# Optimization experiments

Measured on AMD Instinct MI355X. Metric: run time of the kernel, lower is better.

The kernel has to match this reference:

```python
import jax, jax.numpy as jnp
import numpy as np

B, T, C, H = 2, 2048, 1024, 16
HD = C // H  # head_dim = 64


def _apply_rope(x, cos, sin):
    # x: [B, T, H, HD]; cos/sin: [T, HD//2]
    xp = x.reshape(x.shape[:-1] + (HD // 2, 2))  # [B,T,H,HD//2,2]
    x0, x1 = xp[..., 0], xp[..., 1]
    c = cos[None, :, None, :]
    s = sin[None, :, None, :]
    rot = jnp.stack([x0 * c - x1 * s, x0 * s + x1 * c], axis=-1)
    return rot.reshape(x.shape)


def setup_inputs() -> dict:
    key0 = jax.random.key(0)
    ks = jax.random.split(key0, 8)
    query = jax.random.normal(ks[0], (B, T, C), dtype=jnp.float32)
    key_ = jax.random.normal(ks[1], (B, T, C), dtype=jnp.float32)
    value = jax.random.normal(ks[2], (B, T, C), dtype=jnp.float32)
    # standard RoPE angle table: pos * inv_freq, shape [T, HD//2]
    pos = jnp.arange(T, dtype=jnp.float32)
    inv_freq = 1.0 / (10000.0 ** (jnp.arange(0, HD, 2, dtype=jnp.float32) / HD))
    freqs = pos[:, None] * inv_freq[None, :]
    scale = 0.02
    Wq = jax.random.normal(ks[3], (C, C), dtype=jnp.float32) * scale
    Wk = jax.random.normal(ks[4], (C, C), dtype=jnp.float32) * scale
    Wv = jax.random.normal(ks[5], (C, C), dtype=jnp.float32) * scale
    Wo = jax.random.normal(ks[6], (C, C), dtype=jnp.float32) * scale
    return {"query": query, "key": key_, "value": value, "freqs": freqs,
            "Wq": Wq, "Wk": Wk, "Wv": Wv, "Wo": Wo}


def reference(query, key, value, freqs, Wq, Wk, Wv, Wo):
    # torch nn.Linear: y = x @ W.T (no bias)
    Q = query @ Wq.T
    K = key @ Wk.T
    V = value @ Wv.T
    cos = jnp.cos(freqs)
    sin = jnp.sin(freqs)
    Q = _apply_rope(Q.reshape(B, T, H, HD), cos, sin)
    K = _apply_rope(K.reshape(B, T, H, HD), cos, sin)
    V = V.reshape(B, T, H, HD)
    # non-causal SDPA, scale = 1/sqrt(head_dim)
    scores = jnp.einsum('bthd,bshd->bhts', Q, K) / jnp.sqrt(jnp.float32(HD))
    probs = jax.nn.softmax(scores, axis=-1)
    y = jnp.einsum('bhts,bshd->bthd', probs, V).reshape(B, T, C)
    return y @ Wo.T
```

## Files before the change

### kernel.cpp

```cpp
#include <hip/hip_runtime.h>
#include <stdint.h>

#define Bd 2
#define Td 2048
#define Cd 1024
#define Hd 16
#define HDd 64
#define BT 4096

typedef _Float16 f16;
typedef __attribute__((ext_vector_type(8))) _Float16 f16x8;
typedef __attribute__((ext_vector_type(4))) _Float16 f16x4;
typedef __attribute__((ext_vector_type(2))) _Float16 f16x2;
typedef __attribute__((ext_vector_type(4))) float f32x4;
typedef __attribute__((ext_vector_type(16))) float f32x16;
typedef __attribute__((ext_vector_type(2))) unsigned uint2v;

#define GLD_LDS16(gptr, lptr)                                                        \
    __builtin_amdgcn_global_load_lds((const __attribute__((address_space(1))) void*)(gptr), \
                                     (__attribute__((address_space(3))) void*)(lptr), 16, 0, 0)

#define MAX3(a, b, c) fmaxf(fmaxf(a, b), c)
#define EXP2(x) __builtin_amdgcn_exp2f(x)

__device__ __forceinline__ float2 xhalf_pair(float v) {
    uint2v r = __builtin_amdgcn_permlane32_swap(__float_as_uint(v), __float_as_uint(v), false, false);
    unsigned lo = r[0], hi = r[1];
    float2 out;
    out.x = __uint_as_float(lo);
    out.y = __uint_as_float(hi);
    return out;
}

__global__ void k_cvt(const float* __restrict__ q, const float* __restrict__ k,
                      const float* __restrict__ v, const float* __restrict__ wq,
                      const float* __restrict__ wk, const float* __restrict__ wv,
                      const float* __restrict__ wo, f16* __restrict__ qh, f16* __restrict__ kh,
                      f16* __restrict__ vh, f16* __restrict__ wqh, f16* __restrict__ wkh,
                      f16* __restrict__ wvh, f16* __restrict__ woh,
                      const float* __restrict__ freqs, float2* __restrict__ csT) {
    int g = blockIdx.x * 256 + threadIdx.x;
    if (g >= 4194304) {
        int i = g - 4194304;
        float f = freqs[i];
        float2 cs;
        cs.x = cosf(f);
        cs.y = sinf(f);
        csT[i] = cs;
        return;
    }
    const float* src;
    f16* dst;
    int base;
    if (g < 1048576)      { src = q;  dst = qh;  base = 0; }
    else if (g < 2097152) { src = k;  dst = kh;  base = 1048576; }
    else if (g < 3145728) { src = v;  dst = vh;  base = 2097152; }
    else if (g < 3407872) { src = wq; dst = wqh; base = 3145728; }
    else if (g < 3670016) { src = wk; dst = wkh; base = 3407872; }
    else if (g < 3932160) { src = wv; dst = wvh; base = 3670016; }
    else                  { src = wo; dst = woh; base = 3932160; }
    int i = g - base;
    float4 val = reinterpret_cast<const float4*>(src)[i];
    f16x4 o;
    o[0] = (f16)val.x; o[1] = (f16)val.y; o[2] = (f16)val.z; o[3] = (f16)val.w;
    reinterpret_cast<f16x4*>(dst)[i] = o;
}

#define GEMM_MAINLOOP(A, W)                                                                  \
    const int tid = threadIdx.x;                                                             \
    const int lane = tid & 63, w = tid >> 6;                                                 \
    const int g = lane >> 4, r15 = lane & 15;                                                \
    const int m0 = blockIdx.x * 128, n0 = blockIdx.y * 128;                                  \
    const int wm = (w >> 1) * 64, wn = (w & 1) * 64;                                         \
    const f32x4 zero4 = {0.f, 0.f, 0.f, 0.f};                                                \
    f32x4 acc[4][4];                                                                         \
    _Pragma("unroll") for (int i = 0; i < 4; ++i) {                                          \
        _Pragma("unroll") for (int j = 0; j < 4; ++j) acc[i][j] = zero4;                     \
    }                                                                                        \
    const int srow0 = tid >> 3;                                                              \
    const int sj = tid & 7;                                                                  \
    for (int k0 = 0; k0 < Cd; k0 += 64) {                                                    \
        _Pragma("unroll") for (int c = 0; c < 4; ++c) {                                      \
            int row = c * 32 + srow0;                                                        \
            int ch = sj ^ (row & 7);                                                         \
            GLD_LDS16(A + (m0 + row) * Cd + k0 + ch * 8, Alds + (c * 256 + w * 64) * 8);     \
            GLD_LDS16(W + (n0 + row) * Cd + k0 + ch * 8, Blds + (c * 256 + w * 64) * 8);     \
        }                                                                                    \
        __syncthreads();                                                                     \
        _Pragma("unroll") for (int half = 0; half < 2; ++half) {                             \
            f16x8 af[4], bf[4];                                                              \
            _Pragma("unroll") for (int t = 0; t < 4; ++t) {                                  \
                int cidx = ((half << 2) | g) ^ (r15 & 7);                                    \
                af[t] = *(const f16x8*)&Alds[(wm + t * 16 + r15) * 64 + cidx * 8];           \
                bf[t] = *(const f16x8*)&Blds[(wn + t * 16 + r15) * 64 + cidx * 8];           \
            }                                                                                \
            _Pragma("unroll") for (int i = 0; i < 4; ++i) {                                  \
                _Pragma("unroll") for (int j = 0; j < 4; ++j) acc[i][j] =                    \
                    __builtin_amdgcn_mfma_f32_16x16x32_f16(af[i], bf[j], acc[i][j], 0, 0, 0); \
            }                                                                                \
        }                                                                                    \
        __syncthreads();                                                                     \
    }

__global__ __launch_bounds__(256, 3) void k_gemm_qkv(
    const f16* __restrict__ qh, const f16* __restrict__ kh, const f16* __restrict__ vh,
    const f16* __restrict__ wqh, const f16* __restrict__ wkh, const f16* __restrict__ wvh,
    f16* __restrict__ Qp, f16* __restrict__ Kp, f16* __restrict__ Vt,
    const float2* __restrict__ csT) {
    __shared__ __attribute__((aligned(16))) char smem[34816];
    f16* Alds = (f16*)smem;
    f16* Blds = (f16*)(smem + 16384);
    const int z = blockIdx.z;
    const f16* A = (z == 0) ? qh : (z == 1) ? kh : vh;
    const f16* W = (z == 0) ? wqh : (z == 1) ? wkh : wvh;
    GEMM_MAINLOOP(A, W)
    if (z < 2) {
        f16* outp = z ? Kp : Qp;
#pragma unroll
        for (int i = 0; i < 4; ++i) {
#pragma unroll
            for (int j = 0; j < 4; ++j) {
#pragma unroll
                for (int r = 0; r < 4; ++r) {
                    int row = m0 + wm + i * 16 + g * 4 + r;
                    int col = n0 + wn + j * 16 + r15;
                    float own = acc[i][j][r];
                    float par = __shfl_xor(own, 1, 64);
                    float2 cs = csT[(row & 2047) * 32 + ((j * 16 + r15) >> 1)];
                    float val = (r15 & 1) ? fmaf(par, cs.y, own * cs.x)
                                          : fmaf(own, cs.x, -par * cs.y);
                    outp[row * Cd + col] = (f16)val;
                }
            }
        }
    } else {
        f16* Clds = (f16*)smem;
#pragma unroll
        for (int i = 0; i < 4; ++i) {
#pragma unroll
            for (int j = 0; j < 4; ++j) {
                f16x4 pv;
#pragma unroll
                for (int r = 0; r < 4; ++r) pv[r] = (f16)acc[i][j][r];
                *(f16x4*)&Clds[(wn + j * 16 + r15) * 136 + wm + i * 16 + g * 4] = pv;
            }
        }
        __syncthreads();
        const int orow = tid >> 1;
        const int th = (tid & 1) * 64;
        const int gcol = n0 + orow;
        const int hh = gcol >> 6, dd = gcol & 63;
        const int bb = m0 >> 11;
        f16* dst = Vt + ((bb * 16 + hh) * 64 + dd) * 2048 + (m0 & 2047) + th;
#pragma unroll
        for (int c = 0; c < 8; ++c) {
            f16x8 vv = *(const f16x8*)&Clds[orow * 136 + th + c * 8];
            *(f16x8*)&dst[c * 8] = vv;
        }
    }
}

__global__ __launch_bounds__(256, 4) void k_gemm_out(const f16* __restrict__ yh,
                                                     const f16* __restrict__ woh,
                                                     float* __restrict__ out) {
    __shared__ __attribute__((aligned(16))) f16 Alds[128 * 64];
    __shared__ __attribute__((aligned(16))) f16 Blds[64 * 64];
    const int tid = threadIdx.x;
    const int lane = tid & 63, w = tid >> 6;
    const int g = lane >> 4, r15 = lane & 15;
    const int m0 = blockIdx.x * 128, n0 = blockIdx.y * 64;
    const int wm = (w >> 1) * 64, wn = (w & 1) * 32;
    const f32x4 zero4 = {0.f, 0.f, 0.f, 0.f};
    f32x4 acc[4][2];
#pragma unroll
    for (int i = 0; i < 4; ++i) {
#pragma unroll
        for (int j = 0; j < 2; ++j) acc[i][j] = zero4;
    }
    const int srow0 = tid >> 3;
    const int sj = tid & 7;
    for (int k0 = 0; k0 < Cd; k0 += 64) {
#pragma unroll
        for (int c = 0; c < 4; ++c) {
            int row = c * 32 + srow0;
            int ch = sj ^ (row & 7);
            GLD_LDS16(yh + (m0 + row) * Cd + k0 + ch * 8, (f16*)Alds + (c * 256 + w * 64) * 8);
        }
#pragma unroll
        for (int c = 0; c < 2; ++c) {
            int row = c * 32 + srow0;
            int ch = sj ^ (row & 7);
            GLD_LDS16(woh + (n0 + row) * Cd + k0 + ch * 8, (f16*)Blds + (c * 256 + w * 64) * 8);
        }
        __syncthreads();
#pragma unroll
        for (int half = 0; half < 2; ++half) {
            f16x8 af[4], bf[2];
            int cidx = ((half << 2) | g) ^ (r15 & 7);
#pragma unroll
            for (int t = 0; t < 4; ++t)
                af[t] = *(const f16x8*)&Alds[(wm + t * 16 + r15) * 64 + cidx * 8];
#pragma unroll
            for (int t = 0; t < 2; ++t)
                bf[t] = *(const f16x8*)&Blds[(wn + t * 16 + r15) * 64 + cidx * 8];
#pragma unroll
            for (int i = 0; i < 4; ++i) {
#pragma unroll
                for (int j = 0; j < 2; ++j)
                    acc[i][j] =
                        __builtin_amdgcn_mfma_f32_16x16x32_f16(af[i], bf[j], acc[i][j], 0, 0, 0);
            }
        }
        __syncthreads();
    }
#pragma unroll
    for (int i = 0; i < 4; ++i) {
#pragma unroll
        for (int j = 0; j < 2; ++j) {
#pragma unroll
            for (int r = 0; r < 4; ++r) {
                int row = m0 + wm + i * 16 + g * 4 + r;
                int col = n0 + wn + j * 16 + r15;
                out[row * Cd + col] = acc[i][j][r];
            }
        }
    }
}

__global__ __launch_bounds__(512, 4) void k_flash(const f16* __restrict__ Qp,
                                                  const f16* __restrict__ Kp,
                                                  const f16* __restrict__ Vt,
                                                  f16* __restrict__ y) {
    __shared__ __attribute__((aligned(16))) f16 Klds[2 * 2 * 4096];
    __shared__ __attribute__((aligned(16))) f16 Vlds[2 * 2 * 4096];
    const int bh = blockIdx.x, b = bh >> 4, h = bh & 15;
    const int tid = threadIdx.x, lane = tid & 63, w = tid >> 6;
    const int r31 = lane & 31, hi = lane >> 5;
    const int g2 = w >> 2, qw = w & 3;

    const int srow = tid >> 3, sj = tid & 7;
    const f16* gK = Kp + (b * 2048 + srow) * 1024 + h * 64 + ((sj ^ (srow & 7)) * 8);
    const f16* gV = Vt + (bh * 64 + srow) * 2048 + ((sj ^ (srow & 7)) * 8);
    f16* lK = (f16*)Klds + w * 512;
    f16* lV = (f16*)Vlds + w * 512;

#define STAGE_PAIR(pb, pi)                                          \
    do {                                                            \
        GLD_LDS16(gK + (2 * (pi)) * 65536, lK + (pb) * 8192);       \
        GLD_LDS16(gK + (2 * (pi) + 1) * 65536, lK + (pb) * 8192 + 4096); \
        GLD_LDS16(gV + (2 * (pi)) * 64, lV + (pb) * 8192);          \
        GLD_LDS16(gV + (2 * (pi) + 1) * 64, lV + (pb) * 8192 + 4096);   \
    } while (0)

    const int qrow = b * 2048 + blockIdx.y * 128 + qw * 32 + r31;
    f16x8 qf[4];
    {
        const f16* qb = Qp + qrow * 1024 + h * 64 + hi * 8;
        const f16 sc = (f16)(0.125f * 1.44269504088896f);
#pragma unroll
        for (int dc = 0; dc < 4; ++dc) {
            f16x8 v = *(const f16x8*)(qb + dc * 16);
#pragma unroll
            for (int j = 0; j < 8; ++j) v[j] = v[j] * sc;
            qf[dc] = v;
        }
    }

    f32x16 o0, o1;
#pragma unroll
    for (int r = 0; r < 16; ++r) { o0[r] = 0.f; o1[r] = 0.f; }
    float m = -1e30f, l = 0.f;

    STAGE_PAIR(0, 0);

    for (int it = 0; it < 16; ++it) {
        __builtin_amdgcn_s_barrier();
        if (it < 15) {
            STAGE_PAIR((it + 1) & 1, it + 1);
            asm volatile("s_waitcnt vmcnt(4)" ::: "memory");
        } else {
            asm volatile("s_waitcnt vmcnt(0)" ::: "memory");
        }
        __builtin_amdgcn_sched_barrier(0);
        __builtin_amdgcn_s_barrier();
        const f16* Kb = (const f16*)Klds + (it & 1) * 8192 + g2 * 4096;
        const f16* Vb = (const f16*)Vlds + (it & 1) * 8192 + g2 * 4096;

        f32x16 s0, s1;
#pragma unroll
        for (int r = 0; r < 16; ++r) { s0[r] = 0.f; s1[r] = 0.f; }
        __builtin_amdgcn_s_setprio(1);
#pragma unroll
        for (int dc = 0; dc < 4; ++dc) {
            int j = (2 * dc + hi) ^ (r31 & 7);
            f16x8 k0 = *(const f16x8*)&Kb[r31 * 64 + j * 8];
            f16x8 k1 = *(const f16x8*)&Kb[(32 + r31) * 64 + j * 8];
            s0 = __builtin_amdgcn_mfma_f32_32x32x16_f16(k0, qf[dc], s0, 0, 0, 0);
            s1 = __builtin_amdgcn_mfma_f32_32x32x16_f16(k1, qf[dc], s1, 0, 0, 0);
        }
        __builtin_amdgcn_s_setprio(0);

        float t16[16];
#pragma unroll
        for (int r = 0; r < 16; ++r) t16[r] = fmaxf(s0[r], s1[r]);
        float p0 = MAX3(t16[0], t16[1], t16[2]);
        float p1 = MAX3(t16[3], t16[4], t16[5]);
        float p2 = MAX3(t16[6], t16[7], t16[8]);
        float p3 = MAX3(t16[9], t16[10], t16[11]);
        float p4 = MAX3(t16[12], t16[13], t16[14]);
        float pmax = fmaxf(MAX3(p0, p1, p2), MAX3(p3, p4, t16[15]));
        {
            float2 pm = xhalf_pair(pmax);
            pmax = fmaxf(pm.x, pm.y);
        }
        if (__any(pmax > m + 8.0f)) {
            float mn = fmaxf(m, pmax);
            float cr = EXP2(m - mn);
            m = mn;
            l *= cr;
#pragma unroll
            for (int r = 0; r < 16; ++r) { o0[r] *= cr; o1[r] *= cr; }
        }
#pragma unroll
        for (int r = 0; r < 16; ++r) s0[r] = EXP2(s0[r] - m);
#pragma unroll
        for (int r = 0; r < 16; ++r) s1[r] = EXP2(s1[r] - m);
        float a16[16];
#pragma unroll
        for (int r = 0; r < 16; ++r) a16[r] = s0[r] + s1[r];
#pragma unroll
        for (int r = 0; r < 8; ++r) a16[r] += a16[r + 8];
#pragma unroll
        for (int r = 0; r < 4; ++r) a16[r] += a16[r + 4];
        float rs = (a16[0] + a16[1]) + (a16[2] + a16[3]);

        unsigned pk[16];
#pragma unroll
        for (int i = 0; i < 8; ++i) {
            auto ha = __builtin_amdgcn_cvt_pkrtz(s0[2 * i], s0[2 * i + 1]);
            __builtin_memcpy(&pk[i], &ha, 4);
            auto hb = __builtin_amdgcn_cvt_pkrtz(s1[2 * i], s1[2 * i + 1]);
            __builtin_memcpy(&pk[8 + i], &hb, 4);
        }

        __builtin_amdgcn_s_setprio(1);
#pragma unroll
        for (int s = 0; s < 4; ++s) {
            const int base = (s >> 1) * 8 + (s & 1) * 4;
            uint2v r0 = __builtin_amdgcn_permlane32_swap(pk[base + 0], pk[base + 2], false, false);
            uint2v r1 = __builtin_amdgcn_permlane32_swap(pk[base + 1], pk[base + 3], false, false);
            union { unsigned u[4]; f16x8 v; } uv;
            uv.u[0] = r0[0];
            uv.u[1] = r1[0];
            uv.u[2] = r0[1];
            uv.u[3] = r1[1];
            int j = (2 * s + hi) ^ (r31 & 7);
            f16x8 v0 = *(const f16x8*)&Vb[r31 * 64 + j * 8];
            f16x8 v1 = *(const f16x8*)&Vb[(32 + r31) * 64 + j * 8];
            o0 = __builtin_amdgcn_mfma_f32_32x32x16_f16(v0, uv.v, o0, 0, 0, 0);
            o1 = __builtin_amdgcn_mfma_f32_32x32x16_f16(v1, uv.v, o1, 0, 0, 0);
        }
        __builtin_amdgcn_s_setprio(0);

        {
            float2 rp = xhalf_pair(rs);
            l += rp.x + rp.y;
        }
    }
#undef STAGE_PAIR

    __syncthreads();
    float* Ko = (float*)Klds;
    float* Vm = (float*)Vlds;
    if (w >= 4) {
        const int slot = ((w - 4) * 64 + lane) * 32;
#pragma unroll
        for (int c = 0; c < 4; ++c) {
            f32x4 t;
#pragma unroll
            for (int i = 0; i < 4; ++i) t[i] = o0[c * 4 + i];
            *(f32x4*)&Ko[slot + c * 4] = t;
#pragma unroll
            for (int i = 0; i < 4; ++i) t[i] = o1[c * 4 + i];
            *(f32x4*)&Ko[slot + 16 + c * 4] = t;
        }
        Vm[((w - 4) * 64 + lane) * 2] = m;
        Vm[((w - 4) * 64 + lane) * 2 + 1] = l;
    }
    __syncthreads();
    if (w < 4) {
        const int slot = (w * 64 + lane) * 32;
        float mB = Vm[(w * 64 + lane) * 2];
        float lB = Vm[(w * 64 + lane) * 2 + 1];
        float mS = fmaxf(m, mB);
        float sA = EXP2(m - mS), sB = EXP2(mB - mS);
        float linv = 1.0f / (l * sA + lB * sB);
        sA *= linv;
        sB *= linv;
        f16* yb = y + qrow * 1024 + h * 64 + hi * 4;
#pragma unroll
        for (int rg = 0; rg < 4; ++rg) {
            f32x4 pB0 = *(const f32x4*)&Ko[slot + rg * 4];
            f32x4 pB1 = *(const f32x4*)&Ko[slot + 16 + rg * 4];
            f16x4 ov;
#pragma unroll
            for (int i = 0; i < 4; ++i) ov[i] = (f16)(o0[rg * 4 + i] * sA + pB0[i] * sB);
            *(f16x4*)&yb[rg * 8] = ov;
#pragma unroll
            for (int i = 0; i < 4; ++i) ov[i] = (f16)(o1[rg * 4 + i] * sA + pB1[i] * sB);
            *(f16x4*)&yb[32 + rg * 8] = ov;
        }
    }
}

extern "C" void kernel_launch(void* const* d_in, const int* in_sizes, int n_in, void* d_out,
                              int out_size, void* d_ws, size_t ws_size, hipStream_t stream) {
    const float* q = (const float*)d_in[0];
    const float* k = (const float*)d_in[1];
    const float* v = (const float*)d_in[2];
    const float* fr = (const float*)d_in[3];
    const float* wq = (const float*)d_in[4];
    const float* wk = (const float*)d_in[5];
    const float* wv = (const float*)d_in[6];
    const float* wo = (const float*)d_in[7];
    char* ws = (char*)d_ws;

    float2* csT = (float2*)(ws + 0);
    f16* qh = (f16*)(ws + 524288);
    f16* kh = (f16*)(ws + 8912896);
    f16* vh = (f16*)(ws + 17301504);
    f16* wqh = (f16*)(ws + 25690112);
    f16* wkh = (f16*)(ws + 27787264);
    f16* wvh = (f16*)(ws + 29884416);
    f16* woh = (f16*)(ws + 31981568);
    f16* Qp = (f16*)(ws + 34078720);
    f16* Kp = (f16*)(ws + 42467328);
    f16* Vt = (f16*)(ws + 50855936);
    f16* yh = (f16*)(ws + 8912896);

    k_cvt<<<16640, 256, 0, stream>>>(q, k, v, wq, wk, wv, wo, qh, kh, vh, wqh, wkh, wvh, woh,
                                     fr, csT);
    dim3 gqkv(32, 8, 3);
    k_gemm_qkv<<<gqkv, 256, 0, stream>>>(qh, kh, vh, wqh, wkh, wvh, Qp, Kp, Vt, csT);
    dim3 gf(32, 16);
    k_flash<<<gf, 512, 0, stream>>>(Qp, Kp, Vt, yh);
    dim3 go(32, 16);
    k_gemm_out<<<go, 256, 0, stream>>>(yh, woh, (float*)d_out);
}
```

Measured before the change: 124.2 us.

## Drop KV-split in flash kernel: 256-thread blocks iterate all keys, single V buffer

The flash attention kernel previously split the key range between two groups of four waves and merged partial outputs through LDS at the end. Now each 256-thread block has four waves that walk all 32 key tiles of 64. K is double-buffered and V is single-buffered, with an extra barrier before the PV step. This removes the cross-wave merge and halves LDS per block so more blocks can be resident. In exchange each wave runs twice as many serial iterations, and V loads are exposed within each iteration.

```diff
diff --git a/kernel.cpp b/kernel.cpp
--- a/kernel.cpp
+++ b/kernel.cpp
@@ -227,16 +227,15 @@
     }
 }
 
-__global__ __launch_bounds__(512, 4) void k_flash(const f16* __restrict__ Qp,
+__global__ __launch_bounds__(256, 6) void k_flash(const f16* __restrict__ Qp,
                                                   const f16* __restrict__ Kp,
                                                   const f16* __restrict__ Vt,
                                                   f16* __restrict__ y) {
-    __shared__ __attribute__((aligned(16))) f16 Klds[2 * 2 * 4096];
-    __shared__ __attribute__((aligned(16))) f16 Vlds[2 * 2 * 4096];
+    __shared__ __attribute__((aligned(16))) f16 Klds[2 * 4096];
+    __shared__ __attribute__((aligned(16))) f16 Vlds[4096];
     const int bh = blockIdx.x, b = bh >> 4, h = bh & 15;
     const int tid = threadIdx.x, lane = tid & 63, w = tid >> 6;
     const int r31 = lane & 31, hi = lane >> 5;
-    const int g2 = w >> 2, qw = w & 3;
 
     const int srow = tid >> 3, sj = tid & 7;
     const f16* gK = Kp + (b * 2048 + srow) * 1024 + h * 64 + ((sj ^ (srow & 7)) * 8);
@@ -244,15 +243,18 @@
     f16* lK = (f16*)Klds + w * 512;
     f16* lV = (f16*)Vlds + w * 512;
 
-#define STAGE_PAIR(pb, pi)                                          \
-    do {                                                            \
-        GLD_LDS16(gK + (2 * (pi)) * 65536, lK + (pb) * 8192);       \
-        GLD_LDS16(gK + (2 * (pi) + 1) * 65536, lK + (pb) * 8192 + 4096); \
-        GLD_LDS16(gV + (2 * (pi)) * 64, lV + (pb) * 8192);          \
-        GLD_LDS16(gV + (2 * (pi) + 1) * 64, lV + (pb) * 8192 + 4096);   \
+#define STAGE_K(pb, j)                                               \
+    do {                                                             \
+        GLD_LDS16(gK + (j) * 65536, lK + (pb) * 4096);               \
+        GLD_LDS16(gK + (j) * 65536 + 32768, lK + (pb) * 4096 + 2048); \
     } while (0)
-
-    const int qrow = b * 2048 + blockIdx.y * 128 + qw * 32 + r31;
+#define STAGE_V(j)                                  \
+    do {                                            \
+        GLD_LDS16(gV + (j) * 64, lV);               \
+        GLD_LDS16(gV + (j) * 64 + 65536, lV + 2048); \
+    } while (0)
+
+    const int qrow = b * 2048 + blockIdx.y * 128 + w * 32 + r31;
     f16x8 qf[4];
     {
         const f16* qb = Qp + qrow * 1024 + h * 64 + hi * 8;
@@ -271,20 +273,15 @@
     for (int r = 0; r < 16; ++r) { o0[r] = 0.f; o1[r] = 0.f; }
     float m = -1e30f, l = 0.f;
 
-    STAGE_PAIR(0, 0);
-
-    for (int it = 0; it < 16; ++it) {
-        __builtin_amdgcn_s_barrier();
-        if (it < 15) {
-            STAGE_PAIR((it + 1) & 1, it + 1);
-            asm volatile("s_waitcnt vmcnt(4)" ::: "memory");
-        } else {
-            asm volatile("s_waitcnt vmcnt(0)" ::: "memory");
-        }
+    STAGE_K(0, 0);
+
+    for (int t = 0; t < 32; ++t) {
+        asm volatile("s_waitcnt vmcnt(0)" ::: "memory");
         __builtin_amdgcn_sched_barrier(0);
         __builtin_amdgcn_s_barrier();
-        const f16* Kb = (const f16*)Klds + (it & 1) * 8192 + g2 * 4096;
-        const f16* Vb = (const f16*)Vlds + (it & 1) * 8192 + g2 * 4096;
+        STAGE_V(t);
+        if (t < 31) STAGE_K((t + 1) & 1, t + 1);
+        const f16* Kb = (const f16*)Klds + (t & 1) * 4096;
 
         f32x16 s0, s1;
 #pragma unroll
@@ -343,6 +340,14 @@
             __builtin_memcpy(&pk[8 + i], &hb, 4);
         }
 
+        if (t < 31) {
+            asm volatile("s_waitcnt vmcnt(2)" ::: "memory");
+        } else {
+            asm volatile("s_waitcnt vmcnt(0)" ::: "memory");
+        }
+        __builtin_amdgcn_sched_barrier(0);
+        __builtin_amdgcn_s_barrier();
+
         __builtin_amdgcn_s_setprio(1);
 #pragma unroll
         for (int s = 0; s < 4; ++s) {
@@ -355,8 +360,8 @@
             uv.u[2] = r0[1];
             uv.u[3] = r1[1];
             int j = (2 * s + hi) ^ (r31 & 7);
-            f16x8 v0 = *(const f16x8*)&Vb[r31 * 64 + j * 8];
-            f16x8 v1 = *(const f16x8*)&Vb[(32 + r31) * 64 + j * 8];
+            f16x8 v0 = *(const f16x8*)&Vlds[r31 * 64 + j * 8];
+            f16x8 v1 = *(const f16x8*)&Vlds[(32 + r31) * 64 + j * 8];
             o0 = __builtin_amdgcn_mfma_f32_32x32x16_f16(v0, uv.v, o0, 0, 0, 0);
             o1 = __builtin_amdgcn_mfma_f32_32x32x16_f16(v1, uv.v, o1, 0, 0, 0);
         }
@@ -367,49 +372,20 @@
             l += rp.x + rp.y;
         }
     }
-#undef STAGE_PAIR
-
-    __syncthreads();
-    float* Ko = (float*)Klds;
-    float* Vm = (float*)Vlds;
-    if (w >= 4) {
-        const int slot = ((w - 4) * 64 + lane) * 32;
-#pragma unroll
-        for (int c = 0; c < 4; ++c) {
-            f32x4 t;
-#pragma unroll
-            for (int i = 0; i < 4; ++i) t[i] = o0[c * 4 + i];
-            *(f32x4*)&Ko[slot + c * 4] = t;
-#pragma unroll
-            for (int i = 0; i < 4; ++i) t[i] = o1[c * 4 + i];
-            *(f32x4*)&Ko[slot + 16 + c * 4] = t;
-        }
-        Vm[((w - 4) * 64 + lane) * 2] = m;
-        Vm[((w - 4) * 64 + lane) * 2 + 1] = l;
-    }
-    __syncthreads();
-    if (w < 4) {
-        const int slot = (w * 64 + lane) * 32;
-        float mB = Vm[(w * 64 + lane) * 2];
-        float lB = Vm[(w * 64 + lane) * 2 + 1];
-        float mS = fmaxf(m, mB);
-        float sA = EXP2(m - mS), sB = EXP2(mB - mS);
-        float linv = 1.0f / (l * sA + lB * sB);
-        sA *= linv;
-        sB *= linv;
-        f16* yb = y + qrow * 1024 + h * 64 + hi * 4;
-#pragma unroll
-        for (int rg = 0; rg < 4; ++rg) {
-            f32x4 pB0 = *(const f32x4*)&Ko[slot + rg * 4];
-            f32x4 pB1 = *(const f32x4*)&Ko[slot + 16 + rg * 4];
-            f16x4 ov;
-#pragma unroll
-            for (int i = 0; i < 4; ++i) ov[i] = (f16)(o0[rg * 4 + i] * sA + pB0[i] * sB);
-            *(f16x4*)&yb[rg * 8] = ov;
-#pragma unroll
-            for (int i = 0; i < 4; ++i) ov[i] = (f16)(o1[rg * 4 + i] * sA + pB1[i] * sB);
-            *(f16x4*)&yb[32 + rg * 8] = ov;
-        }
+#undef STAGE_K
+#undef STAGE_V
+
+    float inv = 1.0f / l;
+    f16* yb = y + qrow * 1024 + h * 64 + hi * 4;
+#pragma unroll
+    for (int rg = 0; rg < 4; ++rg) {
+        f16x4 ov;
+#pragma unroll
+        for (int i = 0; i < 4; ++i) ov[i] = (f16)(o0[rg * 4 + i] * inv);
+        *(f16x4*)&yb[rg * 8] = ov;
+#pragma unroll
+        for (int i = 0; i < 4; ++i) ov[i] = (f16)(o1[rg * 4 + i] * inv);
+        *(f16x4*)&yb[32 + rg * 8] = ov;
     }
 }
 
@@ -443,7 +419,7 @@
     dim3 gqkv(32, 8, 3);
     k_gemm_qkv<<<gqkv, 256, 0, stream>>>(qh, kh, vh, wqh, wkh, wvh, Qp, Kp, Vt, csT);
     dim3 gf(32, 16);
-    k_flash<<<gf, 512, 0, stream>>>(Qp, Kp, Vt, yh);
+    k_flash<<<gf, 256, 0, stream>>>(Qp, Kp, Vt, yh);
     dim3 go(32, 16);
     k_gemm_out<<<go, 256, 0, stream>>>(yh, woh, (float*)d_out);
 }
```

Result: slower. 224.1 us (+80.5%).
